# Kernel optimization log

Measured on AMD Instinct MI355X. Metric: run time of the kernel, lower is better.

Reference implementation:

```python
import jax, jax.numpy as jnp
import numpy as np

F = 32          # conf['num_features']
G = 96          # voxel grid extent
N_VOX = 80000   # occupied input voxels
BN_EPS = 1e-5


def _encode(c):
    c = c.astype(np.int64) + 8
    return (c[:, 0] * 512 + c[:, 1]) * 512 + c[:, 2]


def _offsets(ks, dil):
    r = np.arange(-(ks // 2), ks // 2 + 1) * dil
    return np.stack(np.meshgrid(r, r, r, indexing='ij'), -1).reshape(-1, 3)


def _build_map(in_coords, out_coords, offsets):
    # For each kernel offset k and output voxel j, find input voxel index at
    # out_coords[j] + offsets[k]; sentinel = n_in / n_out when absent.
    n_in, n_out = len(in_coords), len(out_coords)
    keys = _encode(in_coords)
    order = np.argsort(keys).astype(np.int32)
    skeys = keys[order]
    K = len(offsets)
    in_map = np.full((K, n_out), n_in, np.int32)
    out_map = np.full((K, n_out), n_out, np.int32)
    base = np.arange(n_out, dtype=np.int32)
    for k, off in enumerate(offsets):
        q = _encode(out_coords + off)
        pos = np.clip(np.searchsorted(skeys, q), 0, n_in - 1)
        valid = skeys[pos] == q
        in_map[k] = np.where(valid, order[pos], n_in)
        out_map[k] = np.where(valid, base, n_out)
    return jnp.asarray(in_map), jnp.asarray(out_map)


def setup_inputs() -> dict:
    rng = np.random.default_rng(0)
    idx = rng.choice(G ** 3, size=N_VOX, replace=False)
    coords = np.stack(np.unravel_index(idx, (G, G, G)), 1).astype(np.int64)
    c2 = np.unique(coords // 2 * 2, axis=0)   # stride-2 coords (enc1 output)
    c4 = np.unique(coords // 4 * 4, axis=0)   # stride-4 coords (c_out.C)

    m1_in, m1_out = _build_map(coords, c2, _offsets(5, 1))  # k5 s2 conv
    m2_in, m2_out = _build_map(c2, c2, _offsets(3, 2))      # enc1 blocks
    m3_in, m3_out = _build_map(c2, c4, _offsets(3, 2))      # conv2 -> c_out.C
    m4_in, m4_out = _build_map(c4, c4, _offsets(3, 4))      # enc2 blocks

    key = jax.random.key(0)
    ks = jax.random.split(key, 8)
    s = 0.05
    return {
        'x_geo': jax.random.normal(ks[0], (N_VOX, 1), jnp.float32),
        'x_col': jax.random.uniform(ks[1], (N_VOX, 3), jnp.float32),
        'w0': jax.random.normal(ks[2], (125, 4, F), jnp.float32) * s,
        'w_e1': jax.random.normal(ks[3], (2, 2, 27, F, F), jnp.float32) * s,
        'g_e1': jnp.ones((2, 2, F), jnp.float32),
        'b_e1': jnp.zeros((2, 2, F), jnp.float32),
        'w2': jax.random.normal(ks[4], (27, F, 2 * F), jnp.float32) * s,
        'w_e2': jax.random.normal(ks[5], (2, 2, 27, 2 * F, 2 * F), jnp.float32) * s,
        'g_e2': jnp.ones((2, 2, 2 * F), jnp.float32),
        'b_e2': jnp.zeros((2, 2, 2 * F), jnp.float32),
        'm1_in': m1_in, 'm1_out': m1_out,
        'm2_in': m2_in, 'm2_out': m2_out,
        'm3_in': m3_in, 'm3_out': m3_out,
        'm4_in': m4_in, 'm4_out': m4_out,
    }


def sparse_conv(feats, W, in_map, out_map):
    # gather -> GEMM -> scatter per kernel offset (lax.scan over K offsets)
    n_out = out_map.shape[1]
    fpad = jnp.concatenate([feats, jnp.zeros((1, feats.shape[1]), feats.dtype)], 0)
    out0 = jnp.zeros((n_out + 1, W.shape[2]), feats.dtype)
    def step(acc, kmw):
        im, om, w = kmw
        return acc.at[om].add(fpad[im] @ w), None
    out, _ = jax.lax.scan(step, out0, (in_map, out_map, W))
    return out[:n_out]


def batch_norm(x, g, b):
    mu = x.mean(0)
    var = ((x - mu) ** 2).mean(0)
    return (x - mu) * jax.lax.rsqrt(var + BN_EPS) * g + b


def basic_block(x, w, g, b, in_map, out_map):
    # ME BasicBlock: conv-BN-ReLU-conv-BN + residual, ReLU
    y = jax.nn.relu(batch_norm(sparse_conv(x, w[0], in_map, out_map), g[0], b[0]))
    y = batch_norm(sparse_conv(y, w[1], in_map, out_map), g[1], b[1])
    return jax.nn.relu(y + x)


def reference(x_geo, x_col, w0, w_e1, g_e1, b_e1, w2, w_e2, g_e2, b_e2,
              m1_in, m1_out, m2_in, m2_out, m3_in, m3_out, m4_in, m4_out):
    x = jnp.concatenate([x_geo, x_col], axis=1)          # ME.cat -> 4 channels
    x = jax.nn.relu(sparse_conv(x, w0, m1_in, m1_out))   # k5 s2 conv + ReLU
    for i in range(2):                                   # enc1 residual blocks
        x = basic_block(x, w_e1[i], g_e1[i], b_e1[i], m2_in, m2_out)
    x = sparse_conv(x, w2, m3_in, m3_out)                # conv2 onto c_out.C
    for i in range(2):                                   # enc2 residual blocks
        x = basic_block(x, w_e2[i], g_e2[i], b_e2[i], m4_in, m4_out)
    return x
```

## Files before the change

kernel.cpp:

```cpp
#include <hip/hip_runtime.h>
#include <hip/hip_bf16.h>


typedef float f4 __attribute__((ext_vector_type(4)));
typedef short short8 __attribute__((ext_vector_type(8)));
typedef short short4v __attribute__((ext_vector_type(4)));

#define BN_EPS 1e-5f

static inline int ceil_div(int a, int b) { return (a + b - 1) / b; }

static __device__ inline float btof(short s) {
    unsigned u = ((unsigned)(unsigned short)s) << 16;
    float f;
    __builtin_memcpy(&f, &u, 4);
    return f;
}
static __device__ inline short ftob(float f) {
    __hip_bfloat16 h = __float2bfloat16(f);
    short s;
    __builtin_memcpy(&s, &h, 2);
    return s;
}

struct Seg {
    const float* W;
    long long begin, end;
    int K, CIN, COUT;
};

struct ProArgs {
    Seg s[10];
    const float* geo;
    const float* col;
    __hip_bfloat16* x0;
    int n_vox;
    float* stats;
    __hip_bfloat16* pads[5];
    int padn[5];
    long long wf_total;
    long long pro_total;
    __hip_bfloat16* Wf;
    const int* m1;
    __hip_bfloat16* A;
    int nc2;
};

template <int C>
__device__ inline void bn_coef(const float* st, const float* g, const float* b,
                               int c, int n, float& sc, float& sh) {
    float rn = 1.f / (float)n;
    float sum = st[c] + st[2 * C + c] + st[4 * C + c] + st[6 * C + c];
    float sq  = st[C + c] + st[3 * C + c] + st[5 * C + c] + st[7 * C + c];
    float mu = sum * rn;
    float inv = rsqrtf(sq * rn - mu * mu + BN_EPS);
    sc = inv * g[c];
    sh = b[c] - mu * sc;
}

__global__ __launch_bounds__(256) void k_prologue(ProArgs pa) {
    for (long long e = (long long)blockIdx.x * 256 + threadIdx.x; e < pa.pro_total;
         e += (long long)gridDim.x * 256) {
        if (e < pa.wf_total) {
            int si = 0;
#pragma unroll
            for (int i = 0; i < 10; ++i)
                if (e >= pa.s[i].end) si = i + 1;
            const Seg sg = pa.s[si];
            long long r = e - sg.begin;
            int j = (int)(r & 7);
            int lane = (int)((r >> 3) & 63);
            long long rest = r >> 9;
            int NT = sg.COUT >> 4;
            int ntile = (int)(rest % NT);
            int chunk = (int)(rest / NT);
            int kd = chunk * 32 + ((lane >> 4) << 3) + j;
            int koff = kd / sg.CIN;
            int ci = kd % sg.CIN;
            int n = ntile * 16 + (lane & 15);
            float v = (koff < sg.K) ? sg.W[((size_t)koff * sg.CIN + ci) * sg.COUT + n] : 0.f;
            pa.Wf[e] = __float2bfloat16(v);
            continue;
        }
        long long r = e - pa.wf_total;
        if (r < pa.n_vox) {
            int row = (int)r;
            pa.x0[row * 4 + 0] = __float2bfloat16(pa.geo[row]);
            pa.x0[row * 4 + 1] = __float2bfloat16(pa.col[row * 3 + 0]);
            pa.x0[row * 4 + 2] = __float2bfloat16(pa.col[row * 3 + 1]);
            pa.x0[row * 4 + 3] = __float2bfloat16(pa.col[row * 3 + 2]);
            continue;
        }
        r -= pa.n_vox;
        if (r < 4096) {
            pa.stats[r] = 0.f;
            continue;
        }
        r -= 4096;
#pragma unroll
        for (int i = 0; i < 5; ++i) {
            if (r < pa.padn[i]) {
                pa.pads[i][r] = __float2bfloat16(0.f);
                r = -1;
                break;
            }
            r -= pa.padn[i];
        }
    }
}

__global__ __launch_bounds__(256) void k_stem(ProArgs a) {
    const int t = threadIdx.x, w = t >> 6, lane = t & 63;
    const int quad = lane >> 4, ml = lane & 15;
    const int ntile = w & 1, mgroup = w >> 1;
    const int n_out = a.nc2, n_in = a.n_vox;
    const __hip_bfloat16* feat = a.x0;
    const __hip_bfloat16* Wf = a.Wf;
    const int* in_map = a.m1;
    __hip_bfloat16* out = a.A;
    const int mb = blockIdx.x * 64 + mgroup * 32;
    const int m0 = mb + ml, m1 = mb + 16 + ml;
    const bool v0 = m0 < n_out, v1 = m1 < n_out;
    f4 acc0 = {0.f, 0.f, 0.f, 0.f};
    f4 acc1 = {0.f, 0.f, 0.f, 0.f};
#pragma unroll 2
    for (int chunk = 0; chunk < 16; ++chunk) {
        int k0 = chunk * 8 + quad * 2;
        int k1 = k0 + 1;
        int k0c = (k0 < 125) ? k0 : 0;
        int k1c = (k1 < 125) ? k1 : 0;
        short8 b = *(const short8*)(Wf + ((size_t)(chunk * 2 + ntile) * 64 + lane) * 8);
        int ia = v0 ? in_map[(size_t)k0c * n_out + m0] : n_in;
        int ib = v0 ? in_map[(size_t)k1c * n_out + m0] : n_in;
        int ic = v1 ? in_map[(size_t)k0c * n_out + m1] : n_in;
        int id = v1 ? in_map[(size_t)k1c * n_out + m1] : n_in;
        short4v p0 = *(const short4v*)(feat + (size_t)ia * 4);
        short4v p1 = *(const short4v*)(feat + (size_t)ib * 4);
        short4v p2 = *(const short4v*)(feat + (size_t)ic * 4);
        short4v p3 = *(const short4v*)(feat + (size_t)id * 4);
        short8 a0, a1;
        a0[0] = p0[0]; a0[1] = p0[1]; a0[2] = p0[2]; a0[3] = p0[3];
        a0[4] = p1[0]; a0[5] = p1[1]; a0[6] = p1[2]; a0[7] = p1[3];
        a1[0] = p2[0]; a1[1] = p2[1]; a1[2] = p2[2]; a1[3] = p2[3];
        a1[4] = p3[0]; a1[5] = p3[1]; a1[6] = p3[2]; a1[7] = p3[3];
        acc0 = __builtin_amdgcn_mfma_f32_16x16x32_bf16(a0, b, acc0, 0, 0, 0);
        acc1 = __builtin_amdgcn_mfma_f32_16x16x32_bf16(a1, b, acc1, 0, 0, 0);
    }
    const int col = ntile * 16 + ml;
#pragma unroll
    for (int i = 0; i < 4; ++i) {
        int r0 = mb + quad * 4 + i;
        if (r0 < n_out)
            out[(size_t)r0 * 32 + col] = __float2bfloat16(fmaxf(acc0[i], 0.f));
        int r1 = mb + 16 + quad * 4 + i;
        if (r1 < n_out)
            out[(size_t)r1 * 32 + col] = __float2bfloat16(fmaxf(acc1[i], 0.f));
    }
}

template <int CIN, int COUT, int MT, int K, bool BNF>
__global__ __launch_bounds__(256, 3) void k_conv(
    const __hip_bfloat16* __restrict__ feat,
    const __hip_bfloat16* __restrict__ Wf,
    const int* __restrict__ in_map,
    __hip_bfloat16* __restrict__ out,
    float* __restrict__ stats,
    const float* __restrict__ in_stats,
    const float* __restrict__ in_g,
    const float* __restrict__ in_b,
    int n_out, int n_in) {
    constexpr int NT = COUT / 16;
    constexpr int H = CIN / 32;
    constexpr int R = MT * 16;
    constexpr int KPW = (K + 3) / 4;
    constexpr int SP = COUT + 1;
    constexpr int D = (MT == 1) ? 4 : 2;
    const int t = threadIdx.x, w = t >> 6, lane = t & 63;
    const int quad = lane >> 4, ml = lane & 15;
    const int mb = blockIdx.x * R;

    __shared__ float red[4 * R * SP];
    __shared__ float sred[2 * 256];
    __shared__ float ibn[2 * CIN];

    if constexpr (BNF) {
        if (t < CIN) {
            float sc, sh;
            bn_coef<CIN>(in_stats, in_g, in_b, t, n_in, sc, sh);
            ibn[t] = sc;
            ibn[CIN + t] = sh;
        }
        __syncthreads();
    }
    float scr[H][8], shr[H][8];
    if constexpr (BNF) {
#pragma unroll
        for (int h = 0; h < H; ++h)
#pragma unroll
            for (int j = 0; j < 8; ++j) {
                int ch = h * 32 + quad * 8 + j;
                scr[h][j] = ibn[ch];
                shr[h][j] = ibn[CIN + ch];
            }
    }

    int idx[KPW][MT];
#pragma unroll
    for (int kk = 0; kk < KPW; ++kk) {
        const int k = kk * 4 + w;
        const int krow = (k < K) ? k : 0;
        const int* mk = in_map + (size_t)krow * n_out;
#pragma unroll
        for (int mi = 0; mi < MT; ++mi) {
            int m = mb + mi * 16 + ml;
            idx[kk][mi] = (m < n_out) ? mk[m] : n_in;
        }
    }

    f4 acc[MT * NT];
#pragma unroll
    for (int i = 0; i < MT * NT; ++i) acc[i] = (f4){0.f, 0.f, 0.f, 0.f};

    short8 av[KPW][MT * H];
#pragma unroll
    for (int s = 0; s < D && s < KPW; ++s)
#pragma unroll
        for (int mi = 0; mi < MT; ++mi)
#pragma unroll
            for (int h = 0; h < H; ++h)
                av[s][mi * H + h] = *(const short8*)(
                    feat + (size_t)idx[s][mi] * CIN + h * 32 + quad * 8);

#pragma unroll
    for (int kk = 0; kk < KPW; ++kk) {
        if (kk + D < KPW) {
#pragma unroll
            for (int mi = 0; mi < MT; ++mi)
#pragma unroll
                for (int h = 0; h < H; ++h)
                    av[kk + D][mi * H + h] = *(const short8*)(
                        feat + (size_t)idx[kk + D][mi] * CIN + h * 32 + quad * 8);
        }
        const int k = kk * 4 + w;
        short8 bfrag[H * NT];
#pragma unroll
        for (int h = 0; h < H; ++h)
#pragma unroll
            for (int nt = 0; nt < NT; ++nt)
                bfrag[h * NT + nt] = *(const short8*)(
                    Wf + (((size_t)(k * H + h) * NT + nt) * 64 + lane) * 8);
#pragma unroll
        for (int mi = 0; mi < MT; ++mi) {
            const bool sent = (idx[kk][mi] == n_in);
#pragma unroll
            for (int h = 0; h < H; ++h) {
                short8 a = av[kk][mi * H + h];
                if constexpr (BNF) {
#pragma unroll
                    for (int j = 0; j < 8; ++j) {
                        float f = btof(a[j]) * scr[h][j] + shr[h][j];
                        f = fmaxf(f, 0.f);
                        a[j] = sent ? (short)0 : ftob(f);
                    }
                }
#pragma unroll
                for (int nt = 0; nt < NT; ++nt)
                    acc[mi * NT + nt] = __builtin_amdgcn_mfma_f32_16x16x32_bf16(
                        a, bfrag[h * NT + nt], acc[mi * NT + nt], 0, 0, 0);
            }
        }
    }

#pragma unroll
    for (int mi = 0; mi < MT; ++mi)
#pragma unroll
        for (int nt = 0; nt < NT; ++nt)
#pragma unroll
            for (int i = 0; i < 4; ++i)
                red[((size_t)w * R + mi * 16 + quad * 4 + i) * SP + nt * 16 + ml] =
                    acc[mi * NT + nt][i];
    __syncthreads();

    constexpr int E = (R * COUT) / 256;
    constexpr int RSTEP = 256 / COUT;
    const int col = t % COUT;
    const int rg = t / COUT;
    float s = 0.f, s2 = 0.f;
#pragma unroll
    for (int i = 0; i < E; ++i) {
        int r = rg + i * RSTEP;
        float v = red[(0 * R + r) * SP + col] + red[(1 * R + r) * SP + col] +
                  red[(2 * R + r) * SP + col] + red[(3 * R + r) * SP + col];
        s += v;
        s2 += v * v;
        int grow = mb + r;
        if (grow < n_out) out[(size_t)grow * COUT + col] = __float2bfloat16(v);
    }

    if (stats) {
        sred[t] = s;
        sred[256 + t] = s2;
        __syncthreads();
        if (t < 2 * COUT) {
            int c = t % COUT;
            int which = t / COUT;
            float v = 0.f;
#pragma unroll
            for (int j = 0; j < RSTEP; ++j) v += sred[which * 256 + j * COUT + c];
            atomicAdd(&stats[((blockIdx.x & 3) * 2 + which) * COUT + c], v);
        }
    }
}

template <int C, bool F32OUT>
__global__ __launch_bounds__(256) void k_bnres(
    const __hip_bfloat16* __restrict__ y, const __hip_bfloat16* __restrict__ res,
    const float* __restrict__ st, const float* __restrict__ g,
    const float* __restrict__ b, void* outp, int n) {
    __shared__ float ibn[2 * C];
    const int t = threadIdx.x;
    if (t < C) {
        float sc, sh;
        bn_coef<C>(st, g, b, t, n, sc, sh);
        ibn[t] = sc;
        ibn[C + t] = sh;
    }
    __syncthreads();
    long long tot = (long long)n * (C / 8);
    long long i = (long long)blockIdx.x * 256 + t;
    if (i >= tot) return;
    int c0 = (int)(i % (C / 8)) * 8;
    short8 v = *(const short8*)(y + i * 8);
    short8 r = *(const short8*)(res + i * 8);
    if constexpr (F32OUT) {
        float* out = (float*)outp;
        f4 o0, o1;
#pragma unroll
        for (int j = 0; j < 8; ++j) {
            float f = btof(v[j]) * ibn[c0 + j] + ibn[C + c0 + j] + btof(r[j]);
            f = fmaxf(f, 0.f);
            if (j < 4) o0[j] = f; else o1[j - 4] = f;
        }
        *(f4*)(out + i * 8) = o0;
        *(f4*)(out + i * 8 + 4) = o1;
    } else {
        __hip_bfloat16* out = (__hip_bfloat16*)outp;
        short8 o;
#pragma unroll
        for (int j = 0; j < 8; ++j) {
            float f = btof(v[j]) * ibn[c0 + j] + ibn[C + c0 + j] + btof(r[j]);
            o[j] = ftob(fmaxf(f, 0.f));
        }
        *(short8*)(out + i * 8) = o;
    }
}

extern "C" void kernel_launch(void* const* d_in, const int* in_sizes, int n_in_cnt,
                              void* d_out, int out_size, void* d_ws, size_t ws_size,
                              hipStream_t stream) {
    const float* x_geo = (const float*)d_in[0];
    const float* x_col = (const float*)d_in[1];
    const float* w0    = (const float*)d_in[2];
    const float* w_e1  = (const float*)d_in[3];
    const float* g_e1  = (const float*)d_in[4];
    const float* b_e1  = (const float*)d_in[5];
    const float* w2    = (const float*)d_in[6];
    const float* w_e2  = (const float*)d_in[7];
    const float* g_e2  = (const float*)d_in[8];
    const float* b_e2  = (const float*)d_in[9];
    const int* m1 = (const int*)d_in[10];
    const int* m2 = (const int*)d_in[12];
    const int* m3 = (const int*)d_in[14];
    const int* m4 = (const int*)d_in[16];

    const int n_vox = in_sizes[0];
    const int nc2 = in_sizes[10] / 125;
    const int nc4 = in_sizes[14] / 27;
    (void)out_size; (void)ws_size; (void)n_in_cnt;

    char* p = (char*)d_ws;
    auto alloc = [&](size_t bytes) -> char* {
        char* r = p;
        p += (bytes + 255) & ~(size_t)255;
        return r;
    };
    float* stats = (float*)alloc(8 * 512 * sizeof(float));
    __hip_bfloat16* x0 = (__hip_bfloat16*)alloc((size_t)(n_vox + 1) * 4 * 2);
    __hip_bfloat16* A  = (__hip_bfloat16*)alloc((size_t)(nc2 + 1) * 32 * 2);
    __hip_bfloat16* B  = (__hip_bfloat16*)alloc((size_t)(nc2 + 1) * 32 * 2);
    __hip_bfloat16* Cb = (__hip_bfloat16*)alloc((size_t)(nc2 + 1) * 32 * 2);
    __hip_bfloat16* D  = (__hip_bfloat16*)alloc((size_t)(nc4 + 1) * 64 * 2);
    __hip_bfloat16* E  = (__hip_bfloat16*)alloc((size_t)(nc4 + 1) * 64 * 2);
    __hip_bfloat16* Fb = (__hip_bfloat16*)alloc((size_t)(nc4 + 1) * 64 * 2);

    const long long sz_stem = 16LL * 2 * 512;
    const long long sz_e1   = 28LL * 2 * 512;
    const long long sz_c2   = 28LL * 4 * 512;
    const long long sz_e2   = 56LL * 4 * 512;
    const long long wf_total = sz_stem + 4 * sz_e1 + sz_c2 + 4 * sz_e2;
    __hip_bfloat16* Wf = (__hip_bfloat16*)alloc((size_t)wf_total * 2);

    ProArgs pa;
    long long cur = 0;
    auto seg = [&](int i, const float* W, int K, int CIN, int COUT, long long n) {
        pa.s[i].W = W; pa.s[i].K = K; pa.s[i].CIN = CIN; pa.s[i].COUT = COUT;
        pa.s[i].begin = cur; pa.s[i].end = cur + n; cur += n;
    };
    seg(0, w0, 125, 4, 32, sz_stem);
    for (int i = 0; i < 4; ++i)
        seg(1 + i, w_e1 + (size_t)i * 27 * 32 * 32, 27, 32, 32, sz_e1);
    seg(5, w2, 27, 32, 64, sz_c2);
    for (int i = 0; i < 4; ++i)
        seg(6 + i, w_e2 + (size_t)i * 27 * 64 * 64, 27, 64, 64, sz_e2);

    long long off_e1[4], off_e2[4];
    cur = sz_stem;
    for (int i = 0; i < 4; ++i) { off_e1[i] = cur; cur += sz_e1; }
    long long off_c2 = cur; cur += sz_c2;
    for (int i = 0; i < 4; ++i) { off_e2[i] = cur; cur += sz_e2; }

    pa.geo = x_geo; pa.col = x_col; pa.x0 = x0; pa.n_vox = n_vox;
    pa.stats = stats;
    pa.pads[0] = x0 + (size_t)n_vox * 4; pa.padn[0] = 4;
    pa.pads[1] = A + (size_t)nc2 * 32;   pa.padn[1] = 32;
    pa.pads[2] = B + (size_t)nc2 * 32;   pa.padn[2] = 32;
    pa.pads[3] = D + (size_t)nc4 * 64;   pa.padn[3] = 64;
    pa.pads[4] = E + (size_t)nc4 * 64;   pa.padn[4] = 64;
    pa.wf_total = wf_total;
    pa.pro_total = wf_total + n_vox + 4096 + (4 + 32 + 32 + 64 + 64);
    pa.Wf = Wf;
    pa.m1 = m1;
    pa.A = A;
    pa.nc2 = nc2;

    k_prologue<<<ceil_div((int)pa.pro_total, 256), 256, 0, stream>>>(pa);
    k_stem<<<ceil_div(nc2, 64), 256, 0, stream>>>(pa);

    k_conv<32, 32, 4, 27, false><<<ceil_div(nc2, 64), 256, 0, stream>>>(
        A, Wf + off_e1[0], m2, B, stats + 0 * 512,
        nullptr, nullptr, nullptr, nc2, nc2);
    k_conv<32, 32, 4, 27, true><<<ceil_div(nc2, 64), 256, 0, stream>>>(
        B, Wf + off_e1[1], m2, Cb, stats + 1 * 512,
        stats + 0 * 512, g_e1 + 0, b_e1 + 0, nc2, nc2);
    k_bnres<32, false><<<ceil_div(nc2 * 4, 256), 256, 0, stream>>>(
        Cb, A, stats + 1 * 512, g_e1 + 32, b_e1 + 32, A, nc2);

    k_conv<32, 32, 4, 27, false><<<ceil_div(nc2, 64), 256, 0, stream>>>(
        A, Wf + off_e1[2], m2, B, stats + 2 * 512,
        nullptr, nullptr, nullptr, nc2, nc2);
    k_conv<32, 32, 4, 27, true><<<ceil_div(nc2, 64), 256, 0, stream>>>(
        B, Wf + off_e1[3], m2, Cb, stats + 3 * 512,
        stats + 2 * 512, g_e1 + 64, b_e1 + 64, nc2, nc2);
    k_bnres<32, false><<<ceil_div(nc2 * 4, 256), 256, 0, stream>>>(
        Cb, A, stats + 3 * 512, g_e1 + 96, b_e1 + 96, A, nc2);

    k_conv<32, 64, 1, 27, false><<<ceil_div(nc4, 16), 256, 0, stream>>>(
        A, Wf + off_c2, m3, D, nullptr,
        nullptr, nullptr, nullptr, nc4, nc2);

    k_conv<64, 64, 1, 27, false><<<ceil_div(nc4, 16), 256, 0, stream>>>(
        D, Wf + off_e2[0], m4, E, stats + 4 * 512,
        nullptr, nullptr, nullptr, nc4, nc4);
    k_conv<64, 64, 1, 27, true><<<ceil_div(nc4, 16), 256, 0, stream>>>(
        E, Wf + off_e2[1], m4, Fb, stats + 5 * 512,
        stats + 4 * 512, g_e2 + 0, b_e2 + 0, nc4, nc4);
    k_bnres<64, false><<<ceil_div(nc4 * 8, 256), 256, 0, stream>>>(
        Fb, D, stats + 5 * 512, g_e2 + 64, b_e2 + 64, D, nc4);

    k_conv<64, 64, 1, 27, false><<<ceil_div(nc4, 16), 256, 0, stream>>>(
        D, Wf + off_e2[2], m4, E, stats + 6 * 512,
        nullptr, nullptr, nullptr, nc4, nc4);
    k_conv<64, 64, 1, 27, true><<<ceil_div(nc4, 16), 256, 0, stream>>>(
        E, Wf + off_e2[3], m4, Fb, stats + 7 * 512,
        stats + 6 * 512, g_e2 + 128, b_e2 + 128, nc4, nc4);
    k_bnres<64, true><<<ceil_div(nc4 * 8, 256), 256, 0, stream>>>(
        Fb, D, stats + 7 * 512, g_e2 + 192, b_e2 + 192, (float*)d_out, nc4);
}
```

Measured before the change: 315.8 us.

## Stage gathered conv features through LDS via async global_load_lds pipeline

Replaces register-prefetched gathers of input feature rows with direct global-to-LDS async loads into per-wave multi-slot staging buffers. The buffers use an XOR-swizzled layout and are tracked with explicit vmcnt waits, then read back as MFMA operands. The goal is to cut register pressure so occupancy can rise, and launch bounds go from 3 to 4 blocks. The staging buffer shares memory with the reduction scratch. In exchange it re-reads in_map for the sentinel check when BN folding is on, issues dummy loads at the tail, and depends on hand-written wait counts, which adds correctness risk.

```diff
diff --git a/kernel.cpp b/kernel.cpp
--- a/kernel.cpp
+++ b/kernel.cpp
@@ -21,6 +21,26 @@
     short s;
     __builtin_memcpy(&s, &h, 2);
     return s;
+}
+
+static __device__ inline void gl_lds16(const void* g, void* l) {
+    __builtin_amdgcn_global_load_lds(
+        (const __attribute__((address_space(1))) void*)g,
+        (__attribute__((address_space(3))) void*)l, 16, 0, 0);
+}
+
+template <int N>
+static __device__ inline void s_wait_vmcnt() {
+    static_assert(N >= 0 && N <= 8, "vmcnt range");
+    if constexpr (N == 0) asm volatile("s_waitcnt vmcnt(0)" ::: "memory");
+    else if constexpr (N == 1) asm volatile("s_waitcnt vmcnt(1)" ::: "memory");
+    else if constexpr (N == 2) asm volatile("s_waitcnt vmcnt(2)" ::: "memory");
+    else if constexpr (N == 3) asm volatile("s_waitcnt vmcnt(3)" ::: "memory");
+    else if constexpr (N == 4) asm volatile("s_waitcnt vmcnt(4)" ::: "memory");
+    else if constexpr (N == 5) asm volatile("s_waitcnt vmcnt(5)" ::: "memory");
+    else if constexpr (N == 6) asm volatile("s_waitcnt vmcnt(6)" ::: "memory");
+    else if constexpr (N == 7) asm volatile("s_waitcnt vmcnt(7)" ::: "memory");
+    else asm volatile("s_waitcnt vmcnt(8)" ::: "memory");
 }
 
 struct Seg {
@@ -159,7 +179,7 @@
 }
 
 template <int CIN, int COUT, int MT, int K, bool BNF>
-__global__ __launch_bounds__(256, 3) void k_conv(
+__global__ __launch_bounds__(256, 4) void k_conv(
     const __hip_bfloat16* __restrict__ feat,
     const __hip_bfloat16* __restrict__ Wf,
     const int* __restrict__ in_map,
@@ -174,14 +194,27 @@
     constexpr int R = MT * 16;
     constexpr int KPW = (K + 3) / 4;
     constexpr int SP = COUT + 1;
+    constexpr int S = CIN / 8;
+    constexpr int RPI = 64 / S;
+    constexpr int NI = R / RPI;
     constexpr int D = (MT == 1) ? 4 : 2;
+    constexpr int STAGE_B = R * CIN * 2;
+    constexpr int STAGE_TOT = 4 * D * STAGE_B;
+    constexpr int RED_B = 4 * R * SP * 4;
+    constexpr int UNION_B = (STAGE_TOT > RED_B) ? STAGE_TOT : RED_B;
+    constexpr int WAIT_N = (D - 1) * NI;
+
+    __shared__ char smem[UNION_B + 2048 + 512];
+    float* red  = (float*)smem;
+    float* sred = (float*)(smem + UNION_B);
+    float* ibn  = (float*)(smem + UNION_B + 2048);
+
     const int t = threadIdx.x, w = t >> 6, lane = t & 63;
     const int quad = lane >> 4, ml = lane & 15;
     const int mb = blockIdx.x * R;
-
-    __shared__ float red[4 * R * SP];
-    __shared__ float sred[2 * 256];
-    __shared__ float ibn[2 * CIN];
+    char* stw = smem + w * (D * STAGE_B);
+    const int srow = lane / S;
+    const int ssl = lane & (S - 1);
 
     if constexpr (BNF) {
         if (t < CIN) {
@@ -204,16 +237,16 @@
             }
     }
 
-    int idx[KPW][MT];
+    int idxs[KPW][NI];
 #pragma unroll
     for (int kk = 0; kk < KPW; ++kk) {
         const int k = kk * 4 + w;
         const int krow = (k < K) ? k : 0;
         const int* mk = in_map + (size_t)krow * n_out;
 #pragma unroll
-        for (int mi = 0; mi < MT; ++mi) {
-            int m = mb + mi * 16 + ml;
-            idx[kk][mi] = (m < n_out) ? mk[m] : n_in;
+        for (int inst = 0; inst < NI; ++inst) {
+            int m = mb + inst * RPI + srow;
+            idxs[kk][inst] = (m < n_out) ? mk[m] : n_in;
         }
     }
 
@@ -221,27 +254,27 @@
 #pragma unroll
     for (int i = 0; i < MT * NT; ++i) acc[i] = (f4){0.f, 0.f, 0.f, 0.f};
 
-    short8 av[KPW][MT * H];
-#pragma unroll
-    for (int s = 0; s < D && s < KPW; ++s)
-#pragma unroll
-        for (int mi = 0; mi < MT; ++mi)
-#pragma unroll
-            for (int h = 0; h < H; ++h)
-                av[s][mi * H + h] = *(const short8*)(
-                    feat + (size_t)idx[s][mi] * CIN + h * 32 + quad * 8);
+    auto issue = [&](int stg, int slot) {
+#pragma unroll
+        for (int inst = 0; inst < NI; ++inst) {
+            int rg = inst * RPI + srow;
+            int gsl = ssl ^ (rg & (S - 1));
+            const __hip_bfloat16* src =
+                feat + (size_t)idxs[stg][inst] * CIN + gsl * 8;
+            gl_lds16(src, stw + slot * STAGE_B + inst * 1024);
+        }
+    };
+
+#pragma unroll
+    for (int s = 0; s < D; ++s) issue(s, s);
 
 #pragma unroll
     for (int kk = 0; kk < KPW; ++kk) {
-        if (kk + D < KPW) {
-#pragma unroll
-            for (int mi = 0; mi < MT; ++mi)
-#pragma unroll
-                for (int h = 0; h < H; ++h)
-                    av[kk + D][mi * H + h] = *(const short8*)(
-                        feat + (size_t)idx[kk + D][mi] * CIN + h * 32 + quad * 8);
-        }
+        s_wait_vmcnt<WAIT_N>();
+        __builtin_amdgcn_sched_barrier(0);
         const int k = kk * 4 + w;
+        const int slot = kk % D;
+
         short8 bfrag[H * NT];
 #pragma unroll
         for (int h = 0; h < H; ++h)
@@ -249,13 +282,27 @@
             for (int nt = 0; nt < NT; ++nt)
                 bfrag[h * NT + nt] = *(const short8*)(
                     Wf + (((size_t)(k * H + h) * NT + nt) * 64 + lane) * 8);
+
+        int cidx[MT];
+        if constexpr (BNF) {
+            const int krow = (k < K) ? k : 0;
+            const int* mk = in_map + (size_t)krow * n_out;
+#pragma unroll
+            for (int mi = 0; mi < MT; ++mi) {
+                int m = mb + mi * 16 + ml;
+                cidx[mi] = (m < n_out) ? mk[m] : n_in;
+            }
+        }
+
 #pragma unroll
         for (int mi = 0; mi < MT; ++mi) {
-            const bool sent = (idx[kk][mi] == n_in);
 #pragma unroll
             for (int h = 0; h < H; ++h) {
-                short8 a = av[kk][mi * H + h];
+                const int p = (h * 4 + quad) ^ (ml & (S - 1));
+                short8 a = *(const short8*)(
+                    stw + slot * STAGE_B + ((mi * 16 + ml) * CIN + p * 8) * 2);
                 if constexpr (BNF) {
+                    const bool sent = (cidx[mi] == n_in);
 #pragma unroll
                     for (int j = 0; j < 8; ++j) {
                         float f = btof(a[j]) * scr[h][j] + shr[h][j];
@@ -269,7 +316,13 @@
                         a, bfrag[h * NT + nt], acc[mi * NT + nt], 0, 0, 0);
             }
         }
-    }
+
+        __builtin_amdgcn_sched_barrier(0);
+        issue((kk + D < KPW) ? (kk + D) : 0, slot);
+    }
+
+    s_wait_vmcnt<0>();
+    __syncthreads();
 
 #pragma unroll
     for (int mi = 0; mi < MT; ++mi)
```

New measurement: 323.1 us. 1.02x slower.
